# Kernel optimization log

Measured on AMD Instinct MI355X. Metric: run time of the kernel, lower is better.

The kernel has to match this reference:

```python
import jax, jax.numpy as jnp
import numpy as np

D_IN = 3
HID = 256
N_BRANCH = 8
SKIP_IN = (4,)
CSG_TREE = [0, 1, [2, 3], [4, 5, [6, 7]]]
FLAG_CONVEX = True
BETA = 100.0
N_POINTS = 100000

# layer dims: [3, 256*7, 8]; layer whose OUTPUT feeds a skip layer emits 256-3=253
_DIMS = [D_IN] + [HID] * 7 + [N_BRANCH]


def _layer_out_dim(layer):
    if (layer + 1) in SKIP_IN:
        return _DIMS[layer + 1] - D_IN
    return _DIMS[layer + 1]


def setup_inputs() -> dict:
    key = jax.random.key(0)
    keys = jax.random.split(key, 20)
    inp = {"x": jax.random.normal(keys[0], (N_POINTS, D_IN), dtype=jnp.float32)}
    n_layers = len(_DIMS) - 1  # 8 linear layers
    for layer in range(n_layers):
        in_d = _DIMS[layer]
        out_d = _layer_out_dim(layer)
        kw = jax.random.fold_in(keys[1], layer)
        if layer == n_layers - 1:  # geometric init of last layer
            W = (np.sqrt(np.pi) / np.sqrt(in_d)
                 + 1e-5 * jax.random.normal(kw, (in_d, out_d), dtype=jnp.float32))
            b = -1.0 * jnp.ones((out_d,), dtype=jnp.float32)
        else:
            W = (np.sqrt(2.0) / np.sqrt(out_d)) * jax.random.normal(
                kw, (in_d, out_d), dtype=jnp.float32)
            b = jnp.zeros((out_d,), dtype=jnp.float32)
        inp[f"W{layer}"] = W
        inp[f"b{layer}"] = b
    return inp


def _softplus_beta(x):
    return jax.nn.softplus(BETA * x) / BETA


def _csg_combine(vals, ops, cvx_flag):
    # hard CSG tree: one-hot matmul == column gather; recursion is static (trace time)
    idxs = [v for v in ops if not isinstance(v, list)]
    cols = [vals[:, jnp.array(idxs)]]
    for v in ops:
        if isinstance(v, list):
            cols.append(_csg_combine(vals, v, not cvx_flag))
    m = jnp.concatenate(cols, axis=1)
    red = jnp.max if cvx_flag else jnp.min
    return red(m, axis=1, keepdims=True)


def _forward(x, Ws, bs):
    inp = x
    h = x
    n_layers = len(Ws)
    inv_sqrt2 = np.float32(1.0 / np.sqrt(2.0))
    for layer in range(n_layers):
        if layer in SKIP_IN:
            h = jnp.concatenate([h, inp], axis=-1) * inv_sqrt2
        h = h @ Ws[layer] + bs[layer]
        if layer < n_layers - 1:
            h = _softplus_beta(h)
    branch_vals = h  # [N, n_branch]
    hcsg = _csg_combine(branch_vals, CSG_TREE, FLAG_CONVEX)  # [N, 1]
    return jnp.concatenate([hcsg, branch_vals], axis=1)  # flag_output == 0


def reference(x, W0, b0, W1, b1, W2, b2, W3, b3, W4, b4, W5, b5, W6, b6, W7, b7):
    Ws = [W0, W1, W2, W3, W4, W5, W6, W7]
    bs = [b0, b1, b2, b3, b4, b5, b6, b7]
    return _forward(x, Ws, bs)
```

## Files before the change

kernel.cpp:

```cpp
#include <hip/hip_runtime.h>
#include <hip/hip_bf16.h>


using bf16x8 = __attribute__((ext_vector_type(8))) __bf16;
using f32x4  = __attribute__((ext_vector_type(4))) float;

#define LDA 264

#define OFFW0 0
#define OFFW1 8192
#define OFFW2 73728
#define OFFW3 139264
#define OFFW4 204800
#define OFFW5 270336
#define OFFW6 335872
#define OFFW7 401408
#define WSB_BYTE_OFF 811008
#define OFFB7 1792

#define SCALE_T2 144.26950408889634f
#define INV_SQRT2 0.70710678118654752f
#define LN2_100 0.0069314718055994531f

__device__ __forceinline__ float fast_exp2(float x) {
#if __has_builtin(__builtin_amdgcn_exp2f)
    return __builtin_amdgcn_exp2f(x);
#else
    return exp2f(x);
#endif
}
__device__ __forceinline__ float fast_log2(float x) {
#if __has_builtin(__builtin_amdgcn_logf)
    return __builtin_amdgcn_logf(x);
#else
    return log2f(x);
#endif
}

__device__ __forceinline__ float softplus_t2(float t2) {
    float e = fast_exp2(-fabsf(t2));
    float l = fast_log2(1.0f + e);
    return fmaxf(t2, 0.0f) + l;
}

__device__ __forceinline__ unsigned short bf16_rne(float f) {
    unsigned int u = __float_as_uint(f);
    unsigned int r = u + 0x7FFFu + ((u >> 16) & 1u);
    return (unsigned short)(r >> 16);
}

template <int KK, int MODE>
__device__ __forceinline__ void layer_mm(
    const unsigned short* __restrict__ wfrag,
    const float* __restrict__ bias,
    unsigned short* act, const float* xst,
    int wave, int lane)
{
    const int quad = lane >> 4;
    const int l15  = lane & 15;

    f32x4 acc[2][2];
#pragma unroll
    for (int i = 0; i < 2; ++i) {
        const int chb = (wave * 2 + i) * 16 + quad * 4;
        const float4 b4 = *(const float4*)(bias + chb);
#pragma unroll
        for (int nt = 0; nt < 2; ++nt)
            acc[i][nt] = f32x4{b4.x, b4.y, b4.z, b4.w};
    }

#pragma unroll
    for (int kk = 0; kk < KK; ++kk) {
        bf16x8 bfr[2];
#pragma unroll
        for (int nt = 0; nt < 2; ++nt)
            bfr[nt] = *(const bf16x8*)(act + (nt * 16 + l15) * LDA + kk * 32 + quad * 8);
#pragma unroll
        for (int i = 0; i < 2; ++i) {
            const int mt = wave * 2 + i;
            bf16x8 afr = *(const bf16x8*)(wfrag + ((mt * KK + kk) * 64 + lane) * 8);
#pragma unroll
            for (int nt = 0; nt < 2; ++nt)
                acc[i][nt] = __builtin_amdgcn_mfma_f32_16x16x32_bf16(afr, bfr[nt], acc[i][nt], 0, 0, 0);
        }
    }

    __syncthreads();

#pragma unroll
    for (int i = 0; i < 2; ++i) {
        const int chb = (wave * 2 + i) * 16 + quad * 4;
#pragma unroll
        for (int nt = 0; nt < 2; ++nt) {
            const int pt = nt * 16 + l15;
            float vv[4];
#pragma unroll
            for (int r = 0; r < 4; ++r) {
                float s = softplus_t2(acc[i][nt][r]);
                if (MODE == 1) {
                    const int ch = chb + r;
                    if (ch >= 253)
                        s = xst[pt * 4 + (ch - 253)];
                }
                vv[r] = s;
            }
            __hip_bfloat162 p01 = __float22bfloat162_rn(float2{vv[0], vv[1]});
            __hip_bfloat162 p23 = __float22bfloat162_rn(float2{vv[2], vv[3]});
            uint2 pk;
            pk.x = *(unsigned int*)&p01;
            pk.y = *(unsigned int*)&p23;
            *(uint2*)(act + pt * LDA + chb) = pk;
        }
    }

    __syncthreads();
}

__global__ __launch_bounds__(512, 8)
void nhrep_main(const float* __restrict__ x, float* __restrict__ out,
                const unsigned short* __restrict__ wsW,
                const float* __restrict__ wsB, int npts)
{
    __shared__ unsigned short act[32 * LDA];
    __shared__ float xst[32 * 4];
    const int tid  = threadIdx.x;
    const int wave = tid >> 6, lane = tid & 63;
    const int quad = lane >> 4, l15 = lane & 15;
    const int base_pt = blockIdx.x * 32;

    for (int i = tid; i < 32 * 32; i += 512) {
        const int pt = i >> 5, ch = i & 31;
        const int ptg = base_pt + pt;
        float v = 0.0f;
        if (ch < 3 && ptg < npts) v = x[ptg * 3 + ch];
        act[pt * LDA + ch] = bf16_rne(v);
        if (ch < 4) xst[pt * 4 + ch] = (ch < 3) ? v : 0.0f;
    }
    __syncthreads();

    layer_mm<1, 0>(wsW + OFFW0, wsB + 0 * 256, act, xst, wave, lane);
    layer_mm<8, 0>(wsW + OFFW1, wsB + 1 * 256, act, xst, wave, lane);
    layer_mm<8, 0>(wsW + OFFW2, wsB + 2 * 256, act, xst, wave, lane);
    layer_mm<8, 1>(wsW + OFFW3, wsB + 3 * 256, act, xst, wave, lane);
    layer_mm<8, 0>(wsW + OFFW4, wsB + 4 * 256, act, xst, wave, lane);
    layer_mm<8, 0>(wsW + OFFW5, wsB + 5 * 256, act, xst, wave, lane);
    layer_mm<8, 0>(wsW + OFFW6, wsB + 6 * 256, act, xst, wave, lane);

    if (wave < 2) {
        const float4 b4 = *(const float4*)(wsB + OFFB7 + quad * 4);
        f32x4 acc = f32x4{b4.x, b4.y, b4.z, b4.w};
        const unsigned short* w7 = wsW + OFFW7;
#pragma unroll
        for (int kk = 0; kk < 8; ++kk) {
            bf16x8 bfr = *(const bf16x8*)(act + (wave * 16 + l15) * LDA + kk * 32 + quad * 8);
            bf16x8 afr = *(const bf16x8*)(w7 + (kk * 64 + lane) * 8);
            acc = __builtin_amdgcn_mfma_f32_16x16x32_bf16(afr, bfr, acc, 0, 0, 0);
        }
        float u0 = __shfl(acc[0], l15 + 16);
        float u1 = __shfl(acc[1], l15 + 16);
        float u2 = __shfl(acc[2], l15 + 16);
        float u3 = __shfl(acc[3], l15 + 16);
        if (quad == 0) {
            const int ptg = base_pt + wave * 16 + l15;
            if (ptg < npts) {
                const float v0 = acc[0], v1 = acc[1], v2 = acc[2], v3 = acc[3];
                const float v4 = u0, v5 = u1, v6 = u2, v7 = u3;
                const float m23   = fminf(v2, v3);
                const float m67   = fmaxf(v6, v7);
                const float m4567 = fminf(fminf(v4, v5), m67);
                const float h     = fmaxf(fmaxf(v0, v1), fmaxf(m23, m4567));
                float* o = out + (long)ptg * 9;
                o[0] = h;
                o[1] = v0; o[2] = v1; o[3] = v2; o[4] = v3;
                o[5] = v4; o[6] = v5; o[7] = v6; o[8] = v7;
            }
        }
    }
}

struct PackArgs {
    const float* W[8];
    const float* b[8];
};

#define TOTAL_FRAGS 50688
#define TOTAL_BIAS  1808

__global__ void prepack_all(PackArgs args, unsigned short* __restrict__ dstW,
                            float* __restrict__ dstB)
{
    const int t = blockIdx.x * blockDim.x + threadIdx.x;
    const int FB[9]  = {0, 1024, 9216, 17408, 25600, 33792, 41984, 50176, 50688};
    const int KKs[8] = {1, 8, 8, 8, 8, 8, 8, 8};
    const int ind[8] = {3, 256, 256, 256, 256, 256, 256, 256};
    const int outd[8]= {256, 256, 256, 253, 256, 256, 256, 8};

    if (t < TOTAL_FRAGS) {
        int l = 0;
        while (t >= FB[l + 1]) ++l;
        const int f    = t - FB[l];
        const int lane = f & 63;
        const int kk   = (f >> 6) % KKs[l];
        const int mt   = f / (64 * KKs[l]);
        const int o    = mt * 16 + (lane & 15);
        const int kb   = kk * 32 + (lane >> 4) * 8;
        const float* W = args.W[l];
        const int in_d = ind[l], out_d = outd[l];

        unsigned short v[8];
#pragma unroll
        for (int j = 0; j < 8; ++j) {
            const int k = kb + j;
            float w = 0.0f;
            if (k < in_d && o < out_d) {
                float sc = 1.0f;
                if (l == 0) sc = SCALE_T2;
                else if (l == 4) sc = (k < 253) ? INV_SQRT2 : (SCALE_T2 * INV_SQRT2);
                else if (l == 7) sc = LN2_100;
                w = W[k * out_d + o] * sc;
            }
            unsigned int u = __float_as_uint(w);
            v[j] = (unsigned short)((u + 0x7FFFu + ((u >> 16) & 1u)) >> 16);
        }
        uint4 p;
        p.x = (unsigned int)v[0] | ((unsigned int)v[1] << 16);
        p.y = (unsigned int)v[2] | ((unsigned int)v[3] << 16);
        p.z = (unsigned int)v[4] | ((unsigned int)v[5] << 16);
        p.w = (unsigned int)v[6] | ((unsigned int)v[7] << 16);
        *(uint4*)(dstW + (long)t * 8) = p;
    } else if (t < TOTAL_FRAGS + TOTAL_BIAS) {
        const int u = t - TOTAL_FRAGS;
        const int l = (u < 1792) ? (u >> 8) : 7;
        const int idx = (l < 7) ? (u & 255) : (u - 1792);
        const float sc = (l < 7) ? SCALE_T2 : 1.0f;
        dstB[u] = (idx < outd[l]) ? args.b[l][idx] * sc : 0.0f;
    }
}

extern "C" void kernel_launch(void* const* d_in, const int* in_sizes, int n_in,
                              void* d_out, int out_size, void* d_ws, size_t ws_size,
                              hipStream_t stream)
{
    const float* x = (const float*)d_in[0];
    unsigned short* wsW = (unsigned short*)d_ws;
    float* wsB = (float*)((char*)d_ws + WSB_BYTE_OFF);

    PackArgs pa;
    for (int l = 0; l < 8; ++l) {
        pa.W[l] = (const float*)d_in[1 + 2 * l];
        pa.b[l] = (const float*)d_in[2 + 2 * l];
    }
    const int ptot = TOTAL_FRAGS + TOTAL_BIAS;
    prepack_all<<<(ptot + 255) / 256, 256, 0, stream>>>(pa, wsW, wsB);

    const int npts = in_sizes[0] / 3;
    const int nblk = (npts + 31) / 32;
    nhrep_main<<<nblk, 512, 0, stream>>>(x, (float*)d_out, wsW, wsB, npts);
}
```

Measured before the change: 208.4 us.

## Ping-pong activation buffers with XOR-swizzled LDS layout to drop a barrier

Activations now alternate between two shared buffers, so each layer reads one and writes the other. This removes the __syncthreads that separated the MFMA reads from the epilogue writes in every layer. The padded row stride (LDA 264) is replaced by a 512-byte row with a 16-byte-granule XOR swizzle to avoid LDS bank conflicts. In exchange, shared memory per block roughly doubles, which could limit how many blocks fit on a CU.

```diff
diff --git a/kernel.cpp b/kernel.cpp
--- a/kernel.cpp
+++ b/kernel.cpp
@@ -4,8 +4,6 @@
 
 using bf16x8 = __attribute__((ext_vector_type(8))) __bf16;
 using f32x4  = __attribute__((ext_vector_type(4))) float;
-
-#define LDA 264
 
 #define OFFW0 0
 #define OFFW1 8192
@@ -49,15 +47,20 @@
     return (unsigned short)(r >> 16);
 }
 
+__device__ __forceinline__ int sw_addr(int pt, int byte_col) {
+    return pt * 512 + ((((byte_col >> 4) ^ (pt & 7)) << 4) | (byte_col & 15));
+}
+
 template <int KK, int MODE>
 __device__ __forceinline__ void layer_mm(
     const unsigned short* __restrict__ wfrag,
     const float* __restrict__ bias,
-    unsigned short* act, const float* xst,
-    int wave, int lane)
+    const unsigned short* src, unsigned short* dst,
+    const float* xst, int wave, int lane)
 {
     const int quad = lane >> 4;
     const int l15  = lane & 15;
+    const int sw   = l15 & 7;
 
     f32x4 acc[2][2];
 #pragma unroll
@@ -74,7 +77,8 @@
         bf16x8 bfr[2];
 #pragma unroll
         for (int nt = 0; nt < 2; ++nt)
-            bfr[nt] = *(const bf16x8*)(act + (nt * 16 + l15) * LDA + kk * 32 + quad * 8);
+            bfr[nt] = *(const bf16x8*)((const char*)src +
+                        (nt * 16 + l15) * 512 + (((kk * 4 + quad) ^ sw) << 4));
 #pragma unroll
         for (int i = 0; i < 2; ++i) {
             const int mt = wave * 2 + i;
@@ -84,8 +88,6 @@
                 acc[i][nt] = __builtin_amdgcn_mfma_f32_16x16x32_bf16(afr, bfr[nt], acc[i][nt], 0, 0, 0);
         }
     }
-
-    __syncthreads();
 
 #pragma unroll
     for (int i = 0; i < 2; ++i) {
@@ -109,7 +111,7 @@
             uint2 pk;
             pk.x = *(unsigned int*)&p01;
             pk.y = *(unsigned int*)&p23;
-            *(uint2*)(act + pt * LDA + chb) = pk;
+            *(uint2*)((char*)dst + sw_addr(pt, chb * 2)) = pk;
         }
     }
 
@@ -121,7 +123,8 @@
                 const unsigned short* __restrict__ wsW,
                 const float* __restrict__ wsB, int npts)
 {
-    __shared__ unsigned short act[32 * LDA];
+    __shared__ unsigned short actA[32 * 256];
+    __shared__ unsigned short actB[32 * 256];
     __shared__ float xst[32 * 4];
     const int tid  = threadIdx.x;
     const int wave = tid >> 6, lane = tid & 63;
@@ -133,26 +136,28 @@
         const int ptg = base_pt + pt;
         float v = 0.0f;
         if (ch < 3 && ptg < npts) v = x[ptg * 3 + ch];
-        act[pt * LDA + ch] = bf16_rne(v);
+        *(unsigned short*)((char*)actA + sw_addr(pt, ch * 2)) = bf16_rne(v);
         if (ch < 4) xst[pt * 4 + ch] = (ch < 3) ? v : 0.0f;
     }
     __syncthreads();
 
-    layer_mm<1, 0>(wsW + OFFW0, wsB + 0 * 256, act, xst, wave, lane);
-    layer_mm<8, 0>(wsW + OFFW1, wsB + 1 * 256, act, xst, wave, lane);
-    layer_mm<8, 0>(wsW + OFFW2, wsB + 2 * 256, act, xst, wave, lane);
-    layer_mm<8, 1>(wsW + OFFW3, wsB + 3 * 256, act, xst, wave, lane);
-    layer_mm<8, 0>(wsW + OFFW4, wsB + 4 * 256, act, xst, wave, lane);
-    layer_mm<8, 0>(wsW + OFFW5, wsB + 5 * 256, act, xst, wave, lane);
-    layer_mm<8, 0>(wsW + OFFW6, wsB + 6 * 256, act, xst, wave, lane);
+    layer_mm<1, 0>(wsW + OFFW0, wsB + 0 * 256, actA, actB, xst, wave, lane);
+    layer_mm<8, 0>(wsW + OFFW1, wsB + 1 * 256, actB, actA, xst, wave, lane);
+    layer_mm<8, 0>(wsW + OFFW2, wsB + 2 * 256, actA, actB, xst, wave, lane);
+    layer_mm<8, 1>(wsW + OFFW3, wsB + 3 * 256, actB, actA, xst, wave, lane);
+    layer_mm<8, 0>(wsW + OFFW4, wsB + 4 * 256, actA, actB, xst, wave, lane);
+    layer_mm<8, 0>(wsW + OFFW5, wsB + 5 * 256, actB, actA, xst, wave, lane);
+    layer_mm<8, 0>(wsW + OFFW6, wsB + 6 * 256, actA, actB, xst, wave, lane);
 
     if (wave < 2) {
         const float4 b4 = *(const float4*)(wsB + OFFB7 + quad * 4);
         f32x4 acc = f32x4{b4.x, b4.y, b4.z, b4.w};
         const unsigned short* w7 = wsW + OFFW7;
+        const int sw = l15 & 7;
 #pragma unroll
         for (int kk = 0; kk < 8; ++kk) {
-            bf16x8 bfr = *(const bf16x8*)(act + (wave * 16 + l15) * LDA + kk * 32 + quad * 8);
+            bf16x8 bfr = *(const bf16x8*)((const char*)actB +
+                           (wave * 16 + l15) * 512 + (((kk * 4 + quad) ^ sw) << 4));
             bf16x8 afr = *(const bf16x8*)(w7 + (kk * 64 + lane) * 8);
             acc = __builtin_amdgcn_mfma_f32_16x16x32_bf16(afr, bfr, acc, 0, 0, 0);
         }
```

Measured after the change: 248.2 us. 19.1% more time.

## Use hybrid 64-point and 32-point tiles so each weight fragment serves more points

Applied to the files above, without the earlier changes.

The kernel becomes a template over points per block. 1024 blocks handle 64 points each, with each wave computing 4 M-tiles for one 32-point half, and the remaining points use the old 32-point path. Each weight fragment loaded from global/L2 now feeds twice as many MFMAs in the big blocks, which lowers weight traffic per point. In exchange the shared memory per block doubles, register pressure rises from the larger accumulators, and the grid is split unevenly between two block sizes.

```diff
diff --git a/kernel.cpp b/kernel.cpp
--- a/kernel.cpp
+++ b/kernel.cpp
@@ -49,20 +49,24 @@
     return (unsigned short)(r >> 16);
 }
 
-template <int KK, int MODE>
+template <int KK, int MODE, int MT>
 __device__ __forceinline__ void layer_mm(
     const unsigned short* __restrict__ wfrag,
     const float* __restrict__ bias,
     unsigned short* act, const float* xst,
     int wave, int lane)
 {
-    const int quad = lane >> 4;
-    const int l15  = lane & 15;
-
-    f32x4 acc[2][2];
-#pragma unroll
-    for (int i = 0; i < 2; ++i) {
-        const int chb = (wave * 2 + i) * 16 + quad * 4;
+    constexpr int NSTRIP = 16 / MT;
+    const int strip = wave & (NSTRIP - 1);
+    const int pg    = (MT == 4) ? (wave >> 2) : 0;
+    const int quad  = lane >> 4;
+    const int l15   = lane & 15;
+    const int row0  = pg * 32 + l15;
+
+    f32x4 acc[MT][2];
+#pragma unroll
+    for (int i = 0; i < MT; ++i) {
+        const int chb = (strip * MT + i) * 16 + quad * 4;
         const float4 b4 = *(const float4*)(bias + chb);
 #pragma unroll
         for (int nt = 0; nt < 2; ++nt)
@@ -74,10 +78,10 @@
         bf16x8 bfr[2];
 #pragma unroll
         for (int nt = 0; nt < 2; ++nt)
-            bfr[nt] = *(const bf16x8*)(act + (nt * 16 + l15) * LDA + kk * 32 + quad * 8);
-#pragma unroll
-        for (int i = 0; i < 2; ++i) {
-            const int mt = wave * 2 + i;
+            bfr[nt] = *(const bf16x8*)(act + (row0 + nt * 16) * LDA + kk * 32 + quad * 8);
+#pragma unroll
+        for (int i = 0; i < MT; ++i) {
+            const int mt = strip * MT + i;
             bf16x8 afr = *(const bf16x8*)(wfrag + ((mt * KK + kk) * 64 + lane) * 8);
 #pragma unroll
             for (int nt = 0; nt < 2; ++nt)
@@ -88,11 +92,11 @@
     __syncthreads();
 
 #pragma unroll
-    for (int i = 0; i < 2; ++i) {
-        const int chb = (wave * 2 + i) * 16 + quad * 4;
+    for (int i = 0; i < MT; ++i) {
+        const int chb = (strip * MT + i) * 16 + quad * 4;
 #pragma unroll
         for (int nt = 0; nt < 2; ++nt) {
-            const int pt = nt * 16 + l15;
+            const int pt = row0 + nt * 16;
             float vv[4];
 #pragma unroll
             for (int r = 0; r < 4; ++r) {
@@ -116,19 +120,18 @@
     __syncthreads();
 }
 
-__global__ __launch_bounds__(512, 8)
-void nhrep_main(const float* __restrict__ x, float* __restrict__ out,
-                const unsigned short* __restrict__ wsW,
-                const float* __restrict__ wsB, int npts)
-{
-    __shared__ unsigned short act[32 * LDA];
-    __shared__ float xst[32 * 4];
-    const int tid  = threadIdx.x;
+template <int NPT>
+__device__ __forceinline__ void run_net(
+    const float* __restrict__ x, float* __restrict__ out,
+    const unsigned short* __restrict__ wsW, const float* __restrict__ wsB,
+    unsigned short* act, float* xst,
+    int base_pt, int npts, int tid)
+{
+    constexpr int MT = NPT / 16;
     const int wave = tid >> 6, lane = tid & 63;
     const int quad = lane >> 4, l15 = lane & 15;
-    const int base_pt = blockIdx.x * 32;
-
-    for (int i = tid; i < 32 * 32; i += 512) {
+
+    for (int i = tid; i < NPT * 32; i += 512) {
         const int pt = i >> 5, ch = i & 31;
         const int ptg = base_pt + pt;
         float v = 0.0f;
@@ -138,15 +141,15 @@
     }
     __syncthreads();
 
-    layer_mm<1, 0>(wsW + OFFW0, wsB + 0 * 256, act, xst, wave, lane);
-    layer_mm<8, 0>(wsW + OFFW1, wsB + 1 * 256, act, xst, wave, lane);
-    layer_mm<8, 0>(wsW + OFFW2, wsB + 2 * 256, act, xst, wave, lane);
-    layer_mm<8, 1>(wsW + OFFW3, wsB + 3 * 256, act, xst, wave, lane);
-    layer_mm<8, 0>(wsW + OFFW4, wsB + 4 * 256, act, xst, wave, lane);
-    layer_mm<8, 0>(wsW + OFFW5, wsB + 5 * 256, act, xst, wave, lane);
-    layer_mm<8, 0>(wsW + OFFW6, wsB + 6 * 256, act, xst, wave, lane);
-
-    if (wave < 2) {
+    layer_mm<1, 0, MT>(wsW + OFFW0, wsB + 0 * 256, act, xst, wave, lane);
+    layer_mm<8, 0, MT>(wsW + OFFW1, wsB + 1 * 256, act, xst, wave, lane);
+    layer_mm<8, 0, MT>(wsW + OFFW2, wsB + 2 * 256, act, xst, wave, lane);
+    layer_mm<8, 1, MT>(wsW + OFFW3, wsB + 3 * 256, act, xst, wave, lane);
+    layer_mm<8, 0, MT>(wsW + OFFW4, wsB + 4 * 256, act, xst, wave, lane);
+    layer_mm<8, 0, MT>(wsW + OFFW5, wsB + 5 * 256, act, xst, wave, lane);
+    layer_mm<8, 0, MT>(wsW + OFFW6, wsB + 6 * 256, act, xst, wave, lane);
+
+    if (wave < NPT / 16) {
         const float4 b4 = *(const float4*)(wsB + OFFB7 + quad * 4);
         f32x4 acc = f32x4{b4.x, b4.y, b4.z, b4.w};
         const unsigned short* w7 = wsW + OFFW7;
@@ -178,6 +181,22 @@
     }
 }
 
+__global__ __launch_bounds__(512, 8)
+void nhrep_main(const float* __restrict__ x, float* __restrict__ out,
+                const unsigned short* __restrict__ wsW,
+                const float* __restrict__ wsB, int npts, int nbig)
+{
+    __shared__ unsigned short act[64 * LDA];
+    __shared__ float xst[64 * 4];
+    const int b = blockIdx.x;
+    if (b < nbig) {
+        run_net<64>(x, out, wsW, wsB, act, xst, b * 64, npts, threadIdx.x);
+    } else {
+        run_net<32>(x, out, wsW, wsB, act, xst, nbig * 64 + (b - nbig) * 32,
+                    npts, threadIdx.x);
+    }
+}
+
 struct PackArgs {
     const float* W[8];
     const float* b[8];
@@ -254,6 +273,10 @@
     prepack_all<<<(ptot + 255) / 256, 256, 0, stream>>>(pa, wsW, wsB);
 
     const int npts = in_sizes[0] / 3;
-    const int nblk = (npts + 31) / 32;
-    nhrep_main<<<nblk, 512, 0, stream>>>(x, (float*)d_out, wsW, wsB, npts);
-}
+    int nbig = npts / 64;
+    if (nbig > 1024) nbig = 1024;
+    const int rem = npts - nbig * 64;
+    const int nsmall = (rem + 31) / 32;
+    nhrep_main<<<nbig + nsmall, 512, 0, stream>>>(x, (float*)d_out, wsW, wsB,
+                                                  npts, nbig);
+}
```

Result: slower. 257.1 us (+23.4%).

## Keep activations in registers across layers with per-wave full-width MFMA tiles

Applied to the files above, without the earlier changes.

Each wave now computes all 256 output channels for its own 32 points, so the MFMA accumulator layout maps directly onto the next layer's B-fragment once the weight K dimension is permuted in prepack. This removes the LDS activation buffer and its per-layer write/read round trip, and blocks become 256 threads handling 128 points. The cost is much higher register pressure (32 f32x4 accumulators plus 16 bf16x8 fragments), lower occupancy, and every wave streaming the full weight matrix from global/L2.

```diff
diff --git a/kernel.cpp b/kernel.cpp
--- a/kernel.cpp
+++ b/kernel.cpp
@@ -4,8 +4,6 @@
 
 using bf16x8 = __attribute__((ext_vector_type(8))) __bf16;
 using f32x4  = __attribute__((ext_vector_type(4))) float;
-
-#define LDA 264
 
 #define OFFW0 0
 #define OFFW1 8192
@@ -49,127 +47,181 @@
     return (unsigned short)(r >> 16);
 }
 
-template <int KK, int MODE>
-__device__ __forceinline__ void layer_mm(
-    const unsigned short* __restrict__ wfrag,
-    const float* __restrict__ bias,
-    unsigned short* act, const float* xst,
-    int wave, int lane)
-{
-    const int quad = lane >> 4;
-    const int l15  = lane & 15;
-
-    f32x4 acc[2][2];
-#pragma unroll
-    for (int i = 0; i < 2; ++i) {
-        const int chb = (wave * 2 + i) * 16 + quad * 4;
-        const float4 b4 = *(const float4*)(bias + chb);
-#pragma unroll
-        for (int nt = 0; nt < 2; ++nt)
-            acc[i][nt] = f32x4{b4.x, b4.y, b4.z, b4.w};
-    }
-
-#pragma unroll
-    for (int kk = 0; kk < KK; ++kk) {
-        bf16x8 bfr[2];
-#pragma unroll
-        for (int nt = 0; nt < 2; ++nt)
-            bfr[nt] = *(const bf16x8*)(act + (nt * 16 + l15) * LDA + kk * 32 + quad * 8);
-#pragma unroll
-        for (int i = 0; i < 2; ++i) {
-            const int mt = wave * 2 + i;
-            bf16x8 afr = *(const bf16x8*)(wfrag + ((mt * KK + kk) * 64 + lane) * 8);
-#pragma unroll
-            for (int nt = 0; nt < 2; ++nt)
-                acc[i][nt] = __builtin_amdgcn_mfma_f32_16x16x32_bf16(afr, bfr[nt], acc[i][nt], 0, 0, 0);
-        }
-    }
-
-    __syncthreads();
-
-#pragma unroll
-    for (int i = 0; i < 2; ++i) {
-        const int chb = (wave * 2 + i) * 16 + quad * 4;
-#pragma unroll
-        for (int nt = 0; nt < 2; ++nt) {
-            const int pt = nt * 16 + l15;
-            float vv[4];
-#pragma unroll
-            for (int r = 0; r < 4; ++r) {
-                float s = softplus_t2(acc[i][nt][r]);
-                if (MODE == 1) {
-                    const int ch = chb + r;
-                    if (ch >= 253)
-                        s = xst[pt * 4 + (ch - 253)];
-                }
-                vv[r] = s;
+union frag_u {
+    bf16x8 v;
+    unsigned short s[8];
+    uint4 u4;
+};
+
+__device__ __forceinline__ unsigned int bits2(__hip_bfloat162 h) {
+    union { __hip_bfloat162 h; unsigned int u; } c;
+    c.h = h;
+    return c.u;
+}
+
+__device__ __forceinline__ bf16x8 sp_pack(f32x4 a, f32x4 c) {
+    frag_u u;
+    u.u4.x = bits2(__float22bfloat162_rn(float2{softplus_t2(a[0]), softplus_t2(a[1])}));
+    u.u4.y = bits2(__float22bfloat162_rn(float2{softplus_t2(a[2]), softplus_t2(a[3])}));
+    u.u4.z = bits2(__float22bfloat162_rn(float2{softplus_t2(c[0]), softplus_t2(c[1])}));
+    u.u4.w = bits2(__float22bfloat162_rn(float2{softplus_t2(c[2]), softplus_t2(c[3])}));
+    return u.v;
+}
+
+__device__ __forceinline__ void layer_K256(
+    const unsigned short* __restrict__ wl, const float* __restrict__ bias,
+    f32x4 (&acc)[16][2], bf16x8 (&b)[2][8], int q)
+{
+#pragma unroll
+    for (int M = 0; M < 16; ++M) {
+        float4 b4 = *(const float4*)(bias + M * 16 + q * 4);
+        f32x4 bv = {b4.x, b4.y, b4.z, b4.w};
+        acc[M][0] = bv;
+        acc[M][1] = bv;
+    }
+#pragma unroll
+    for (int kk = 0; kk < 8; ++kk) {
+#pragma unroll
+        for (int Mh = 0; Mh < 2; ++Mh) {
+            bf16x8 af[8];
+#pragma unroll
+            for (int mi = 0; mi < 8; ++mi)
+                af[mi] = *(const bf16x8*)(wl + (((Mh * 8 + mi) * 8 + kk) * 512));
+#pragma unroll
+            for (int mi = 0; mi < 8; ++mi) {
+                const int M = Mh * 8 + mi;
+                acc[M][0] = __builtin_amdgcn_mfma_f32_16x16x32_bf16(af[mi], b[0][kk], acc[M][0], 0, 0, 0);
+                acc[M][1] = __builtin_amdgcn_mfma_f32_16x16x32_bf16(af[mi], b[1][kk], acc[M][1], 0, 0, 0);
             }
-            __hip_bfloat162 p01 = __float22bfloat162_rn(float2{vv[0], vv[1]});
-            __hip_bfloat162 p23 = __float22bfloat162_rn(float2{vv[2], vv[3]});
-            uint2 pk;
-            pk.x = *(unsigned int*)&p01;
-            pk.y = *(unsigned int*)&p23;
-            *(uint2*)(act + pt * LDA + chb) = pk;
-        }
-    }
-
-    __syncthreads();
-}
-
-__global__ __launch_bounds__(512, 8)
+        }
+    }
+}
+
+__device__ __forceinline__ void layer_K32(
+    const unsigned short* __restrict__ wl, const float* __restrict__ bias,
+    f32x4 (&acc)[16][2], bf16x8 (&b)[2][8], int q)
+{
+#pragma unroll
+    for (int M = 0; M < 16; ++M) {
+        float4 b4 = *(const float4*)(bias + M * 16 + q * 4);
+        f32x4 bv = {b4.x, b4.y, b4.z, b4.w};
+        acc[M][0] = bv;
+        acc[M][1] = bv;
+    }
+#pragma unroll
+    for (int Mh = 0; Mh < 2; ++Mh) {
+        bf16x8 af[8];
+#pragma unroll
+        for (int mi = 0; mi < 8; ++mi)
+            af[mi] = *(const bf16x8*)(wl + (Mh * 8 + mi) * 512);
+#pragma unroll
+        for (int mi = 0; mi < 8; ++mi) {
+            const int M = Mh * 8 + mi;
+            acc[M][0] = __builtin_amdgcn_mfma_f32_16x16x32_bf16(af[mi], b[0][0], acc[M][0], 0, 0, 0);
+            acc[M][1] = __builtin_amdgcn_mfma_f32_16x16x32_bf16(af[mi], b[1][0], acc[M][1], 0, 0, 0);
+        }
+    }
+}
+
+__device__ __forceinline__ void epilogue(f32x4 (&acc)[16][2], bf16x8 (&b)[2][8]) {
+#pragma unroll
+    for (int nt = 0; nt < 2; ++nt)
+#pragma unroll
+        for (int kk = 0; kk < 8; ++kk)
+            b[nt][kk] = sp_pack(acc[2 * kk][nt], acc[2 * kk + 1][nt]);
+}
+
+__global__ __launch_bounds__(256, 2)
 void nhrep_main(const float* __restrict__ x, float* __restrict__ out,
                 const unsigned short* __restrict__ wsW,
                 const float* __restrict__ wsB, int npts)
 {
-    __shared__ unsigned short act[32 * LDA];
-    __shared__ float xst[32 * 4];
     const int tid  = threadIdx.x;
     const int wave = tid >> 6, lane = tid & 63;
-    const int quad = lane >> 4, l15 = lane & 15;
-    const int base_pt = blockIdx.x * 32;
-
-    for (int i = tid; i < 32 * 32; i += 512) {
-        const int pt = i >> 5, ch = i & 31;
-        const int ptg = base_pt + pt;
-        float v = 0.0f;
-        if (ch < 3 && ptg < npts) v = x[ptg * 3 + ch];
-        act[pt * LDA + ch] = bf16_rne(v);
-        if (ch < 4) xst[pt * 4 + ch] = (ch < 3) ? v : 0.0f;
-    }
+    const int q = lane >> 4, l15 = lane & 15;
+    const int base = blockIdx.x * 128 + wave * 32;
+
+    unsigned short xb[2][3];
+#pragma unroll
+    for (int nt = 0; nt < 2; ++nt) {
+        const int pt = base + nt * 16 + l15;
+        const bool ok = pt < npts;
+#pragma unroll
+        for (int c = 0; c < 3; ++c)
+            xb[nt][c] = ok ? bf16_rne(x[pt * 3 + c]) : (unsigned short)0;
+    }
+
+    bf16x8 b[2][8];
+#pragma unroll
+    for (int nt = 0; nt < 2; ++nt) {
+        frag_u f;
+        f.u4 = uint4{0u, 0u, 0u, 0u};
+        if (q == 0) { f.s[0] = xb[nt][0]; f.s[1] = xb[nt][1]; f.s[2] = xb[nt][2]; }
+        b[nt][0] = f.v;
+#pragma unroll
+        for (int kk = 1; kk < 8; ++kk) {
+            frag_u z;
+            z.u4 = uint4{0u, 0u, 0u, 0u};
+            b[nt][kk] = z.v;
+        }
+    }
+
+    f32x4 acc[16][2];
+
+    layer_K32(wsW + OFFW0 + lane * 8, wsB, acc, b, q);
+    epilogue(acc, b);
     __syncthreads();
 
-    layer_mm<1, 0>(wsW + OFFW0, wsB + 0 * 256, act, xst, wave, lane);
-    layer_mm<8, 0>(wsW + OFFW1, wsB + 1 * 256, act, xst, wave, lane);
-    layer_mm<8, 0>(wsW + OFFW2, wsB + 2 * 256, act, xst, wave, lane);
-    layer_mm<8, 1>(wsW + OFFW3, wsB + 3 * 256, act, xst, wave, lane);
-    layer_mm<8, 0>(wsW + OFFW4, wsB + 4 * 256, act, xst, wave, lane);
-    layer_mm<8, 0>(wsW + OFFW5, wsB + 5 * 256, act, xst, wave, lane);
-    layer_mm<8, 0>(wsW + OFFW6, wsB + 6 * 256, act, xst, wave, lane);
-
-    if (wave < 2) {
-        const float4 b4 = *(const float4*)(wsB + OFFB7 + quad * 4);
-        f32x4 acc = f32x4{b4.x, b4.y, b4.z, b4.w};
-        const unsigned short* w7 = wsW + OFFW7;
+#pragma unroll 1
+    for (int l = 1; l <= 6; ++l) {
+        layer_K256(wsW + OFFW1 + (l - 1) * 65536 + lane * 8, wsB + l * 256, acc, b, q);
+        epilogue(acc, b);
+        if (l == 3) {
+#pragma unroll
+            for (int nt = 0; nt < 2; ++nt) {
+                frag_u f;
+                f.v = b[nt][7];
+                if (q == 3) { f.s[5] = xb[nt][0]; f.s[6] = xb[nt][1]; f.s[7] = xb[nt][2]; }
+                b[nt][7] = f.v;
+            }
+        }
+        __syncthreads();
+    }
+
+    f32x4 a7[2];
+    {
+        float4 b4 = *(const float4*)(wsB + OFFB7 + q * 4);
+        f32x4 bv = {b4.x, b4.y, b4.z, b4.w};
+        a7[0] = bv;
+        a7[1] = bv;
+        const unsigned short* wl = wsW + OFFW7 + lane * 8;
 #pragma unroll
         for (int kk = 0; kk < 8; ++kk) {
-            bf16x8 bfr = *(const bf16x8*)(act + (wave * 16 + l15) * LDA + kk * 32 + quad * 8);
-            bf16x8 afr = *(const bf16x8*)(w7 + (kk * 64 + lane) * 8);
-            acc = __builtin_amdgcn_mfma_f32_16x16x32_bf16(afr, bfr, acc, 0, 0, 0);
-        }
-        float u0 = __shfl(acc[0], l15 + 16);
-        float u1 = __shfl(acc[1], l15 + 16);
-        float u2 = __shfl(acc[2], l15 + 16);
-        float u3 = __shfl(acc[3], l15 + 16);
-        if (quad == 0) {
-            const int ptg = base_pt + wave * 16 + l15;
-            if (ptg < npts) {
-                const float v0 = acc[0], v1 = acc[1], v2 = acc[2], v3 = acc[3];
-                const float v4 = u0, v5 = u1, v6 = u2, v7 = u3;
+            bf16x8 af = *(const bf16x8*)(wl + kk * 512);
+            a7[0] = __builtin_amdgcn_mfma_f32_16x16x32_bf16(af, b[0][kk], a7[0], 0, 0, 0);
+            a7[1] = __builtin_amdgcn_mfma_f32_16x16x32_bf16(af, b[1][kk], a7[1], 0, 0, 0);
+        }
+    }
+
+    float u[2][4];
+#pragma unroll
+    for (int nt = 0; nt < 2; ++nt)
+#pragma unroll
+        for (int r = 0; r < 4; ++r)
+            u[nt][r] = __shfl(a7[nt][r], l15 + 16);
+
+    if (q == 0) {
+#pragma unroll
+        for (int nt = 0; nt < 2; ++nt) {
+            const int pt = base + nt * 16 + l15;
+            if (pt < npts) {
+                const float v0 = a7[nt][0], v1 = a7[nt][1], v2 = a7[nt][2], v3 = a7[nt][3];
+                const float v4 = u[nt][0], v5 = u[nt][1], v6 = u[nt][2], v7 = u[nt][3];
                 const float m23   = fminf(v2, v3);
                 const float m67   = fmaxf(v6, v7);
                 const float m4567 = fminf(fminf(v4, v5), m67);
                 const float h     = fmaxf(fmaxf(v0, v1), fmaxf(m23, m4567));
-                float* o = out + (long)ptg * 9;
+                float* o = out + (long)pt * 9;
                 o[0] = h;
                 o[1] = v0; o[2] = v1; o[3] = v2; o[4] = v3;
                 o[5] = v4; o[6] = v5; o[7] = v6; o[8] = v7;
@@ -203,14 +255,14 @@
         const int kk   = (f >> 6) % KKs[l];
         const int mt   = f / (64 * KKs[l]);
         const int o    = mt * 16 + (lane & 15);
-        const int kb   = kk * 32 + (lane >> 4) * 8;
+        const int q    = lane >> 4;
         const float* W = args.W[l];
         const int in_d = ind[l], out_d = outd[l];
 
         unsigned short v[8];
 #pragma unroll
         for (int j = 0; j < 8; ++j) {
-            const int k = kb + j;
+            const int k = kk * 32 + ((j >> 2) << 4) + (q << 2) + (j & 3);
             float w = 0.0f;
             if (k < in_d && o < out_d) {
                 float sc = 1.0f;
@@ -254,6 +306,6 @@
     prepack_all<<<(ptot + 255) / 256, 256, 0, stream>>>(pa, wsW, wsB);
 
     const int npts = in_sizes[0] / 3;
-    const int nblk = (npts + 31) / 32;
-    nhrep_main<<<nblk, 512, 0, stream>>>(x, (float*)d_out, wsW, wsB, npts);
-}
+    const int nblk = (npts + 127) / 128;
+    nhrep_main<<<nblk, 256, 0, stream>>>(x, (float*)d_out, wsW, wsB, npts);
+}
```

After: 336.4 us. 1.61x slower.
